# Kernel optimization log

Hardware: AMD Instinct MI355X
Metric: run time of the kernel (lower is better)

## Reference

```python
import jax, jax.numpy as jnp
import numpy as np

H_DIM = 768
N_HEADS = 12
SEQ = 4096
MLP_RATIO = 4
EPS = 1e-5


def layernorm(x, g, b):
    mu = jnp.mean(x, axis=-1, keepdims=True)
    var = jnp.var(x, axis=-1, keepdims=True)
    return (x - mu) * jax.lax.rsqrt(var + EPS) * g + b


def setup_inputs() -> dict:
    key = jax.random.key(0)
    ks = jax.random.split(key, 16)
    C, F = H_DIM, MLP_RATIO * H_DIM
    s = 1.0 / np.sqrt(C)
    inp = {
        "x": jax.random.normal(ks[0], (1, SEQ, C), dtype=jnp.float32),
        "Wq": jax.random.normal(ks[1], (C, C), dtype=jnp.float32) * s,
        "bq": jnp.zeros((C,), jnp.float32),
        "Wk": jax.random.normal(ks[2], (C, C), dtype=jnp.float32) * s,
        "bk": jnp.zeros((C,), jnp.float32),
        "Wv": jax.random.normal(ks[3], (C, C), dtype=jnp.float32) * s,
        "bv": jnp.zeros((C,), jnp.float32),
        "Wo": jax.random.normal(ks[4], (C, C), dtype=jnp.float32) * s,
        "bo": jnp.zeros((C,), jnp.float32),
        "ln1_g": jnp.ones((C,), jnp.float32),
        "ln1_b": jnp.zeros((C,), jnp.float32),
        "W1": jax.random.normal(ks[5], (C, F), dtype=jnp.float32) * s,
        "b1": jnp.zeros((F,), jnp.float32),
        "W2": jax.random.normal(ks[6], (F, C), dtype=jnp.float32) * (1.0 / np.sqrt(F)),
        "b2": jnp.zeros((C,), jnp.float32),
        "ln2_g": jnp.ones((C,), jnp.float32),
        "ln2_b": jnp.zeros((C,), jnp.float32),
    }
    return inp


def reference(x, Wq, bq, Wk, bk, Wv, bv, Wo, bo, ln1_g, ln1_b, W1, b1, W2, b2, ln2_g, ln2_b):
    B, T, C = x.shape
    N, D = N_HEADS, C // N_HEADS

    # --- masked self-attention (naive, materializes T x T scores) ---
    q = (x @ Wq + bq).reshape(B, T, N, D).transpose(0, 2, 1, 3)  # [B,N,T,D]
    k = (x @ Wk + bk).reshape(B, T, N, D).transpose(0, 2, 1, 3)
    v = (x @ Wv + bv).reshape(B, T, N, D).transpose(0, 2, 1, 3)

    logits = jnp.einsum("bntd,bnsd->bnts", q, k) / jnp.sqrt(jnp.float32(D))
    causal = jnp.tril(jnp.ones((T, T), dtype=bool))  # True where allowed
    logits = jnp.where(causal, logits, -jnp.inf)
    attn = jax.nn.softmax(logits, axis=-1)
    out = jnp.einsum("bnts,bnsd->bntd", attn, v)
    out = out.transpose(0, 2, 1, 3).reshape(B, T, C)
    attn_out = out @ Wo + bo

    # --- post-norm residual + MLP ---
    h = layernorm(x + attn_out, ln1_g, ln1_b)
    mlp = jax.nn.gelu(h @ W1 + b1, approximate=False) @ W2 + b2
    y = layernorm(h + mlp, ln2_g, ln2_b)
    return y
```

## Files before the change

### kernel.cpp

```cpp
#include <hip/hip_runtime.h>
#include <hip/hip_bf16.h>
#include <math.h>

#define T_SEQ 4096
#define C_DIM 768
#define N_HEADS 12
#define D_HEAD 64
#define F_DIM 3072
#define EPS 1e-5f
#define QSCALE 0.18033688011112042f

typedef __attribute__((ext_vector_type(8))) short short8;
typedef __attribute__((ext_vector_type(4))) float f32x4;

__device__ __forceinline__ void gload_lds16(const void* g, void* lds) {
    __builtin_amdgcn_global_load_lds(
        (const __attribute__((address_space(1))) unsigned int*)g,
        (__attribute__((address_space(3))) unsigned int*)lds, 16, 0, 0);
}

__launch_bounds__(256)
__global__ void transpose_w(const float* __restrict__ W, __hip_bfloat16* __restrict__ Wt,
                            int K, int N) {
    __shared__ float tile[64][65];
    const int k0 = blockIdx.x * 64;
    const int n0 = blockIdx.y * 64;
    const int tid = threadIdx.x;
    const int c = tid & 63;
    const int r0 = (tid >> 6) * 16;
    #pragma unroll
    for (int i = 0; i < 16; ++i)
        tile[r0 + i][c] = W[(size_t)(k0 + r0 + i) * N + n0 + c];
    __syncthreads();
    #pragma unroll
    for (int i = 0; i < 16; ++i)
        Wt[(size_t)(n0 + r0 + i) * K + k0 + c] = __float2bfloat16(tile[c][r0 + i]);
}

__launch_bounds__(256)
__global__ void concat_bias(const float* __restrict__ bq, const float* __restrict__ bk,
                            const float* __restrict__ bv, float* __restrict__ o) {
    const int i = blockIdx.x * 256 + threadIdx.x;
    if (i < C_DIM) {
        o[i] = bq[i];
        o[C_DIM + i] = bk[i];
        o[2 * C_DIM + i] = bv[i];
    }
}

__launch_bounds__(256)
__global__ void f32_to_bf16_vec(const float* __restrict__ in, __hip_bfloat16* __restrict__ out,
                                int n4) {
    const int i = blockIdx.x * 256 + threadIdx.x;
    if (i < n4) {
        const float4 v = *reinterpret_cast<const float4*>(&in[(size_t)i * 4]);
        ushort4 u;
        u.x = __bfloat16_as_ushort(__float2bfloat16(v.x));
        u.y = __bfloat16_as_ushort(__float2bfloat16(v.y));
        u.z = __bfloat16_as_ushort(__float2bfloat16(v.z));
        u.w = __bfloat16_as_ushort(__float2bfloat16(v.w));
        *reinterpret_cast<ushort4*>(&out[(size_t)i * 4]) = u;
    }
}

#define GBM 128
#define GBN 128
#define GBK 64

template<int MODE>
__launch_bounds__(256)
__global__ void gemm_mfma(const __hip_bfloat16* __restrict__ A,
                          const __hip_bfloat16* __restrict__ Bt,
                          const float* __restrict__ bias,
                          float* __restrict__ outf,
                          __hip_bfloat16* __restrict__ outq,
                          __hip_bfloat16* __restrict__ outk,
                          __hip_bfloat16* __restrict__ outvt,
                          int M, int N, int K) {
    __shared__ __hip_bfloat16 As[GBM][GBK];
    __shared__ __hip_bfloat16 Bs[GBN][GBK];

    const int tid = threadIdx.x;
    const int l   = tid & 63;
    const int w   = tid >> 6;
    const int lr  = l & 15;
    const int lg  = l >> 4;
    const int wr  = w >> 1;
    const int wc  = w & 1;
    const int bm  = blockIdx.y * GBM;
    const int bn  = blockIdx.x * GBN;

    const int srow  = l >> 3;
    const int skoff = (l & 7) * 8;

    f32x4 acc[4][4];
    #pragma unroll
    for (int m = 0; m < 4; ++m)
        #pragma unroll
        for (int n = 0; n < 4; ++n)
            acc[m][n] = {0.f, 0.f, 0.f, 0.f};

    for (int k0 = 0; k0 < K; k0 += GBK) {
        if (k0) __syncthreads();
        #pragma unroll
        for (int i = 0; i < 4; ++i) {
            const int rb = (w * 4 + i) * 8;
            gload_lds16(&A[(size_t)(bm + rb + srow) * K + k0 + skoff], &As[rb][0]);
            gload_lds16(&Bt[(size_t)(bn + rb + srow) * K + k0 + skoff], &Bs[rb][0]);
        }
        __syncthreads();

        #pragma unroll
        for (int kk = 0; kk < 2; ++kk) {
            short8 af[4], bf[4];
            #pragma unroll
            for (int m = 0; m < 4; ++m)
                af[m] = *reinterpret_cast<const short8*>(&As[wr * 64 + m * 16 + lr][kk * 32 + lg * 8]);
            #pragma unroll
            for (int n = 0; n < 4; ++n)
                bf[n] = *reinterpret_cast<const short8*>(&Bs[wc * 64 + n * 16 + lr][kk * 32 + lg * 8]);
            #pragma unroll
            for (int m = 0; m < 4; ++m)
                #pragma unroll
                for (int n = 0; n < 4; ++n)
                    acc[m][n] = __builtin_amdgcn_mfma_f32_16x16x32_bf16(af[m], bf[n], acc[m][n], 0, 0, 0);
        }
    }

    #pragma unroll
    for (int m = 0; m < 4; ++m) {
        #pragma unroll
        for (int rr = 0; rr < 4; ++rr) {
            const int row = bm + wr * 64 + m * 16 + lg * 4 + rr;
            #pragma unroll
            for (int n = 0; n < 4; ++n) {
                const int col = bn + wc * 64 + n * 16 + lr;
                float v = acc[m][n][rr] + bias[col];
                if constexpr (MODE == 0) {
                    outf[(size_t)row * N + col] = v;
                } else if constexpr (MODE == 1) {
                    v = 0.5f * v * (1.0f + erff(v * 0.70710678118654752f));
                    outq[(size_t)row * N + col] = __float2bfloat16(v);
                } else {
                    if (col < C_DIM)
                        outq[(size_t)row * C_DIM + col] = __float2bfloat16(v * QSCALE);
                    else if (col < 2 * C_DIM)
                        outk[(size_t)row * C_DIM + (col - C_DIM)] = __float2bfloat16(v);
                    else
                        outvt[(size_t)(col - 2 * C_DIM) * T_SEQ + row] = __float2bfloat16(v);
                }
            }
        }
    }
}

#define QBLK 64
#define KVB 128

__launch_bounds__(256)
__global__ void attn_mfma(const __hip_bfloat16* __restrict__ q,
                          const __hip_bfloat16* __restrict__ k,
                          const __hip_bfloat16* __restrict__ vt,
                          __hip_bfloat16* __restrict__ o) {
    __shared__ __hip_bfloat16 Ks[2][KVB][64];
    __shared__ __hip_bfloat16 Vts[2][D_HEAD][KVB];
    __shared__ __hip_bfloat16 Ps[4][16][KVB];

    const int tid  = threadIdx.x;
    const int wid  = tid >> 6;
    const int lane = tid & 63;
    const int lr   = lane & 15;
    const int lg   = lane >> 4;

    const int h  = blockIdx.x;
    const int q0 = T_SEQ - QBLK - blockIdx.y * QBLK;
    const int qw = q0 + wid * 16;

    const int ksrc = 8 * ((lane & 7) ^ (lane >> 3));
    const int kr   = lane >> 3;
    const int vr   = lane >> 4;
    const int vs   = lane & 15;

    short8 aq[2];
    #pragma unroll
    for (int kk = 0; kk < 2; ++kk)
        aq[kk] = *reinterpret_cast<const short8*>(
            &q[(size_t)(qw + lr) * C_DIM + h * D_HEAD + kk * 32 + lg * 8]);

    f32x4 o_acc[4];
    #pragma unroll
    for (int dc = 0; dc < 4; ++dc) o_acc[dc] = {0.f, 0.f, 0.f, 0.f};
    float m_run[4], l_part[4];
    #pragma unroll
    for (int r = 0; r < 4; ++r) { m_run[r] = -1e30f; l_part[r] = 0.f; }

    auto stage = [&](int buf, int s0) {
        #pragma unroll
        for (int i = 0; i < 4; ++i) {
            const int rb = wid * 32 + i * 8;
            gload_lds16(&k[(size_t)(s0 + rb + kr) * C_DIM + h * D_HEAD + ksrc],
                        &Ks[buf][rb][0]);
        }
        #pragma unroll
        for (int i = 0; i < 4; ++i) {
            const int vb = wid * 16 + i * 4;
            const int vsrc = 8 * (vs ^ (i * 4 + vr));
            gload_lds16(&vt[(size_t)(h * D_HEAD + vb + vr) * T_SEQ + s0 + vsrc],
                        &Vts[buf][vb][0]);
        }
    };

    const int n_tiles = (q0 + QBLK + KVB - 1) / KVB;

    stage(0, 0);
    __syncthreads();

    for (int t = 0; t < n_tiles; ++t) {
        const int cur = t & 1;
        if (t + 1 < n_tiles) stage(cur ^ 1, (t + 1) * KVB);

        f32x4 s_acc[8];
        __builtin_amdgcn_s_setprio(1);
        #pragma unroll
        for (int c = 0; c < 8; ++c) {
            s_acc[c] = {0.f, 0.f, 0.f, 0.f};
            #pragma unroll
            for (int kk = 0; kk < 2; ++kk) {
                const short8 bk8 = *reinterpret_cast<const short8*>(
                    &Ks[cur][c * 16 + lr][8 * ((4 * kk + lg) ^ (lr & 7))]);
                s_acc[c] = __builtin_amdgcn_mfma_f32_16x16x32_bf16(aq[kk], bk8, s_acc[c], 0, 0, 0);
            }
        }
        __builtin_amdgcn_s_setprio(0);

        if (t == n_tiles - 1) {
            const int s0 = t * KVB;
            #pragma unroll
            for (int c = 0; c < 8; ++c)
                #pragma unroll
                for (int r = 0; r < 4; ++r) {
                    const int sg = s0 + c * 16 + lr;
                    const int qg = qw + lg * 4 + r;
                    if (sg > qg) s_acc[c][r] = -1e30f;
                }
        }

        float pm[4];
        #pragma unroll
        for (int r = 0; r < 4; ++r) {
            const float m0 = fmaxf(fmaxf(s_acc[0][r], s_acc[1][r]),
                                   fmaxf(s_acc[2][r], s_acc[3][r]));
            const float m1 = fmaxf(fmaxf(s_acc[4][r], s_acc[5][r]),
                                   fmaxf(s_acc[6][r], s_acc[7][r]));
            pm[r] = fmaxf(m0, m1);
        }
        const float need = fmaxf(fmaxf(pm[0] - m_run[0], pm[1] - m_run[1]),
                                 fmaxf(pm[2] - m_run[2], pm[3] - m_run[3]));
        if (!__all(need <= 8.0f)) {
            #pragma unroll
            for (int r = 0; r < 4; ++r) {
                float nm = pm[r];
                #pragma unroll
                for (int off = 1; off < 16; off <<= 1)
                    nm = fmaxf(nm, __shfl_xor(nm, off));
                nm = fmaxf(nm, m_run[r]);
                const float corr = __builtin_amdgcn_exp2f(m_run[r] - nm);
                m_run[r] = nm;
                l_part[r] *= corr;
                #pragma unroll
                for (int dc = 0; dc < 4; ++dc) o_acc[dc][r] *= corr;
            }
        }
        #pragma unroll
        for (int r = 0; r < 4; ++r) {
            const int qrow = lg * 4 + r;
            float ls = 0.f;
            #pragma unroll
            for (int c = 0; c < 8; ++c) {
                const float pv = __builtin_amdgcn_exp2f(s_acc[c][r] - m_run[r]);
                ls += pv;
                const int slot = (2 * c + (lr >> 3)) ^ qrow;
                Ps[wid][qrow][slot * 8 + (lr & 7)] = __float2bfloat16(pv);
            }
            l_part[r] += ls;
        }

        short8 ap[4];
        #pragma unroll
        for (int kk = 0; kk < 4; ++kk)
            ap[kk] = *reinterpret_cast<const short8*>(
                &Ps[wid][lr][8 * ((4 * kk + lg) ^ lr)]);
        __builtin_amdgcn_s_setprio(1);
        #pragma unroll
        for (int dc = 0; dc < 4; ++dc)
            #pragma unroll
            for (int kk = 0; kk < 4; ++kk) {
                const short8 bv8 = *reinterpret_cast<const short8*>(
                    &Vts[cur][dc * 16 + lr][8 * ((4 * kk + lg) ^ lr)]);
                o_acc[dc] = __builtin_amdgcn_mfma_f32_16x16x32_bf16(ap[kk], bv8, o_acc[dc], 0, 0, 0);
            }
        __builtin_amdgcn_s_setprio(0);

        __syncthreads();
    }

    #pragma unroll
    for (int r = 0; r < 4; ++r) {
        #pragma unroll
        for (int off = 1; off < 16; off <<= 1)
            l_part[r] += __shfl_xor(l_part[r], off);
    }

    #pragma unroll
    for (int dc = 0; dc < 4; ++dc)
        #pragma unroll
        for (int r = 0; r < 4; ++r)
            o[(size_t)(qw + lg * 4 + r) * C_DIM + h * D_HEAD + dc * 16 + lr] =
                __float2bfloat16(o_acc[dc][r] / l_part[r]);
}

template<bool WB16>
__launch_bounds__(256)
__global__ void add_ln(const float* __restrict__ a, const float* __restrict__ b,
                       const float* __restrict__ g, const float* __restrict__ beta,
                       float* __restrict__ outf, __hip_bfloat16* __restrict__ outb) {
    const int row = blockIdx.x;
    const int tid = threadIdx.x;
    const size_t rb = (size_t)row * C_DIM;

    float x[3];
    #pragma unroll
    for (int i = 0; i < 3; ++i) {
        const int c = tid + 256 * i;
        x[i] = a[rb + c] + b[rb + c];
    }

    float s = x[0] + x[1] + x[2];
    float s2 = x[0] * x[0] + x[1] * x[1] + x[2] * x[2];

    #pragma unroll
    for (int off = 32; off; off >>= 1) {
        s  += __shfl_xor(s, off);
        s2 += __shfl_xor(s2, off);
    }

    __shared__ float red[10];
    const int wave = tid >> 6;
    const int lane = tid & 63;
    if (lane == 0) { red[wave] = s; red[4 + wave] = s2; }
    __syncthreads();
    if (tid == 0) {
        const float ts  = red[0] + red[1] + red[2] + red[3];
        const float ts2 = red[4] + red[5] + red[6] + red[7];
        const float mu = ts * (1.0f / C_DIM);
        const float var = ts2 * (1.0f / C_DIM) - mu * mu;
        red[8] = mu;
        red[9] = rsqrtf(var + EPS);
    }
    __syncthreads();
    const float mu = red[8];
    const float rstd = red[9];

    #pragma unroll
    for (int i = 0; i < 3; ++i) {
        const int c = tid + 256 * i;
        const float v = (x[i] - mu) * rstd * g[c] + beta[c];
        outf[rb + c] = v;
        if constexpr (WB16) outb[rb + c] = __float2bfloat16(v);
    }
}

extern "C" void kernel_launch(void* const* d_in, const int* in_sizes, int n_in,
                              void* d_out, int out_size, void* d_ws, size_t ws_size,
                              hipStream_t stream) {
    const float* x     = (const float*)d_in[0];
    const float* Wq    = (const float*)d_in[1];
    const float* bq    = (const float*)d_in[2];
    const float* Wk    = (const float*)d_in[3];
    const float* bk    = (const float*)d_in[4];
    const float* Wv    = (const float*)d_in[5];
    const float* bv    = (const float*)d_in[6];
    const float* Wo    = (const float*)d_in[7];
    const float* bo    = (const float*)d_in[8];
    const float* ln1_g = (const float*)d_in[9];
    const float* ln1_b = (const float*)d_in[10];
    const float* W1    = (const float*)d_in[11];
    const float* b1    = (const float*)d_in[12];
    const float* W2    = (const float*)d_in[13];
    const float* b2    = (const float*)d_in[14];
    const float* ln2_g = (const float*)d_in[15];
    const float* ln2_b = (const float*)d_in[16];

    float* out = (float*)d_out;

    char* wsb = (char*)d_ws;
    const size_t TCb16 = (size_t)T_SEQ * C_DIM * 2;
    __hip_bfloat16* xb  = (__hip_bfloat16*)(wsb);
    __hip_bfloat16* qb  = (__hip_bfloat16*)(wsb + TCb16);
    __hip_bfloat16* kb  = (__hip_bfloat16*)(wsb + 2 * TCb16);
    __hip_bfloat16* vtb = (__hip_bfloat16*)(wsb + 3 * TCb16);
    __hip_bfloat16* mid = (__hip_bfloat16*)(wsb);
    float* proj = (float*)(wsb + 4 * TCb16);
    float* mlpo = proj;
    __hip_bfloat16* obuf = (__hip_bfloat16*)(wsb + 4 * TCb16 + 12582912);
    __hip_bfloat16* hb   = obuf;
    float* hbuf = (float*)(wsb + 4 * TCb16 + 12582912 + TCb16);
    char* we = wsb + 4 * TCb16 + 12582912 + TCb16 + 12582912;
    __hip_bfloat16* Wqkv_t = (__hip_bfloat16*)(we);
    __hip_bfloat16* Wo_t   = (__hip_bfloat16*)(we + 3538944);
    __hip_bfloat16* W1_t   = (__hip_bfloat16*)(we + 3538944 + 1179648);
    __hip_bfloat16* W2_t   = (__hip_bfloat16*)(we + 3538944 + 1179648 + 4718592);
    float* bqkv            = (float*)(we + 3538944 + 1179648 + 2 * 4718592);

    const dim3 blk256(256);

    transpose_w<<<dim3(12, 12), blk256, 0, stream>>>(Wq, Wqkv_t,                   C_DIM, C_DIM);
    transpose_w<<<dim3(12, 12), blk256, 0, stream>>>(Wk, Wqkv_t + (size_t)C_DIM * C_DIM,     C_DIM, C_DIM);
    transpose_w<<<dim3(12, 12), blk256, 0, stream>>>(Wv, Wqkv_t + (size_t)2 * C_DIM * C_DIM, C_DIM, C_DIM);
    transpose_w<<<dim3(12, 12), blk256, 0, stream>>>(Wo, Wo_t, C_DIM, C_DIM);
    transpose_w<<<dim3(12, 48), blk256, 0, stream>>>(W1, W1_t, C_DIM, F_DIM);
    transpose_w<<<dim3(48, 12), blk256, 0, stream>>>(W2, W2_t, F_DIM, C_DIM);
    concat_bias<<<dim3(3), blk256, 0, stream>>>(bq, bk, bv, bqkv);
    f32_to_bf16_vec<<<dim3(3072), blk256, 0, stream>>>(x, xb, T_SEQ * C_DIM / 4);

    gemm_mfma<2><<<dim3(3 * C_DIM / GBN, T_SEQ / GBM), blk256, 0, stream>>>(
        xb, Wqkv_t, bqkv, nullptr, qb, kb, vtb, T_SEQ, 3 * C_DIM, C_DIM);

    attn_mfma<<<dim3(N_HEADS, T_SEQ / QBLK), blk256, 0, stream>>>(qb, kb, vtb, obuf);

    gemm_mfma<0><<<dim3(C_DIM / GBN, T_SEQ / GBM), blk256, 0, stream>>>(
        obuf, Wo_t, bo, proj, nullptr, nullptr, nullptr, T_SEQ, C_DIM, C_DIM);

    add_ln<true><<<dim3(T_SEQ), blk256, 0, stream>>>(x, proj, ln1_g, ln1_b, hbuf, hb);

    gemm_mfma<1><<<dim3(F_DIM / GBN, T_SEQ / GBM), blk256, 0, stream>>>(
        hb, W1_t, b1, nullptr, mid, nullptr, nullptr, T_SEQ, F_DIM, C_DIM);

    gemm_mfma<0><<<dim3(C_DIM / GBN, T_SEQ / GBM), blk256, 0, stream>>>(
        mid, W2_t, b2, mlpo, nullptr, nullptr, nullptr, T_SEQ, C_DIM, F_DIM);

    add_ln<false><<<dim3(T_SEQ), blk256, 0, stream>>>(hbuf, mlpo, ln2_g, ln2_b, out, nullptr);
}
```

Baseline: 366.2 us.

## Double-buffer GEMM LDS tiles and merge four square weight transposes into one launch

The MFMA GEMM now keeps two LDS buffers for A and B tiles and issues the global-to-LDS loads for the next K tile before computing on the current one, so one barrier per iteration replaces two and load latency can overlap with MFMA work. Separately, the four 768x768 weight transposes (Wq, Wk, Wv, Wo) are folded into one kernel launch indexed by blockIdx.z, cutting launch overhead. Doubling LDS to 64KB per block may reduce occupancy. Overlap also relies on the asynchronous LDS loads not being waited on before the compute, which is not guaranteed.

```diff
diff --git a/kernel.cpp b/kernel.cpp
--- a/kernel.cpp
+++ b/kernel.cpp
@@ -17,6 +17,29 @@
     __builtin_amdgcn_global_load_lds(
         (const __attribute__((address_space(1))) unsigned int*)g,
         (__attribute__((address_space(3))) unsigned int*)lds, 16, 0, 0);
+}
+
+__launch_bounds__(256)
+__global__ void transpose_w4(const float* __restrict__ Wq, const float* __restrict__ Wk,
+                             const float* __restrict__ Wv, const float* __restrict__ Wo,
+                             __hip_bfloat16* __restrict__ Wqkv_t,
+                             __hip_bfloat16* __restrict__ Wo_t) {
+    __shared__ float tile[64][65];
+    const int z = blockIdx.z;
+    const float* W = (z == 0) ? Wq : (z == 1) ? Wk : (z == 2) ? Wv : Wo;
+    __hip_bfloat16* Wt = (z < 3) ? (Wqkv_t + (size_t)z * C_DIM * C_DIM) : Wo_t;
+    const int k0 = blockIdx.x * 64;
+    const int n0 = blockIdx.y * 64;
+    const int tid = threadIdx.x;
+    const int c = tid & 63;
+    const int r0 = (tid >> 6) * 16;
+    #pragma unroll
+    for (int i = 0; i < 16; ++i)
+        tile[r0 + i][c] = W[(size_t)(k0 + r0 + i) * C_DIM + n0 + c];
+    __syncthreads();
+    #pragma unroll
+    for (int i = 0; i < 16; ++i)
+        Wt[(size_t)(n0 + r0 + i) * C_DIM + k0 + c] = __float2bfloat16(tile[c][r0 + i]);
 }
 
 __launch_bounds__(256)
@@ -77,8 +100,8 @@
                           __hip_bfloat16* __restrict__ outk,
                           __hip_bfloat16* __restrict__ outvt,
                           int M, int N, int K) {
-    __shared__ __hip_bfloat16 As[GBM][GBK];
-    __shared__ __hip_bfloat16 Bs[GBN][GBK];
+    __shared__ __hip_bfloat16 As[2][GBM][GBK];
+    __shared__ __hip_bfloat16 Bs[2][GBN][GBK];
 
     const int tid = threadIdx.x;
     const int l   = tid & 63;
@@ -100,25 +123,33 @@
         for (int n = 0; n < 4; ++n)
             acc[m][n] = {0.f, 0.f, 0.f, 0.f};
 
-    for (int k0 = 0; k0 < K; k0 += GBK) {
-        if (k0) __syncthreads();
+    auto stage = [&](int buf, int k0) {
         #pragma unroll
         for (int i = 0; i < 4; ++i) {
             const int rb = (w * 4 + i) * 8;
-            gload_lds16(&A[(size_t)(bm + rb + srow) * K + k0 + skoff], &As[rb][0]);
-            gload_lds16(&Bt[(size_t)(bn + rb + srow) * K + k0 + skoff], &Bs[rb][0]);
-        }
+            gload_lds16(&A[(size_t)(bm + rb + srow) * K + k0 + skoff], &As[buf][rb][0]);
+            gload_lds16(&Bt[(size_t)(bn + rb + srow) * K + k0 + skoff], &Bs[buf][rb][0]);
+        }
+    };
+
+    const int nk = K / GBK;
+    stage(0, 0);
+    for (int kt = 0; kt < nk; ++kt) {
+        const int cur = kt & 1;
         __syncthreads();
+        if (kt + 1 < nk) stage(cur ^ 1, (kt + 1) * GBK);
 
         #pragma unroll
         for (int kk = 0; kk < 2; ++kk) {
             short8 af[4], bf[4];
             #pragma unroll
             for (int m = 0; m < 4; ++m)
-                af[m] = *reinterpret_cast<const short8*>(&As[wr * 64 + m * 16 + lr][kk * 32 + lg * 8]);
+                af[m] = *reinterpret_cast<const short8*>(
+                    &As[cur][wr * 64 + m * 16 + lr][kk * 32 + lg * 8]);
             #pragma unroll
             for (int n = 0; n < 4; ++n)
-                bf[n] = *reinterpret_cast<const short8*>(&Bs[wc * 64 + n * 16 + lr][kk * 32 + lg * 8]);
+                bf[n] = *reinterpret_cast<const short8*>(
+                    &Bs[cur][wc * 64 + n * 16 + lr][kk * 32 + lg * 8]);
             #pragma unroll
             for (int m = 0; m < 4; ++m)
                 #pragma unroll
@@ -414,10 +445,7 @@
 
     const dim3 blk256(256);
 
-    transpose_w<<<dim3(12, 12), blk256, 0, stream>>>(Wq, Wqkv_t,                   C_DIM, C_DIM);
-    transpose_w<<<dim3(12, 12), blk256, 0, stream>>>(Wk, Wqkv_t + (size_t)C_DIM * C_DIM,     C_DIM, C_DIM);
-    transpose_w<<<dim3(12, 12), blk256, 0, stream>>>(Wv, Wqkv_t + (size_t)2 * C_DIM * C_DIM, C_DIM, C_DIM);
-    transpose_w<<<dim3(12, 12), blk256, 0, stream>>>(Wo, Wo_t, C_DIM, C_DIM);
+    transpose_w4<<<dim3(12, 12, 4), blk256, 0, stream>>>(Wq, Wk, Wv, Wo, Wqkv_t, Wo_t);
     transpose_w<<<dim3(12, 48), blk256, 0, stream>>>(W1, W1_t, C_DIM, F_DIM);
     transpose_w<<<dim3(48, 12), blk256, 0, stream>>>(W2, W2_t, F_DIM, C_DIM);
     concat_bias<<<dim3(3), blk256, 0, stream>>>(bq, bk, bv, bqkv);
```

Measured after the change: 383.7 us. 1.05x slower.
